# Kernel optimization log

Measured on AMD Instinct MI355X. Metric: run time of the kernel, lower is better.

## Reference

```python
import jax, jax.numpy as jnp
import numpy as np

BN_EPS = 1e-5

def setup_inputs() -> dict:
    key = jax.random.key(0)
    ks = jax.random.split(key, 4)
    B, C, H, W = 8, 64, 128, 128
    return {
        "x": jax.random.normal(ks[0], (B, C, H, W), jnp.float32),
        "w_reduce": jax.random.normal(ks[1], (C, C), jnp.float32) * 0.05,
        "b_reduce": jnp.zeros((C,), jnp.float32),
        "bn_gamma": jnp.ones((C,), jnp.float32),
        "bn_beta": jnp.zeros((C,), jnp.float32),
        "w_span": jax.random.normal(ks[2], (9, C), jnp.float32) * 0.05,
        "b_span": jnp.zeros((9,), jnp.float32),
        "w_conv2": jax.random.normal(ks[3], (C, C, 3, 3), jnp.float32) * 0.02,
        "b_conv2": jnp.zeros((C,), jnp.float32),
    }


def _involution(x, w_reduce, b_reduce, bn_gamma, bn_beta, w_span, b_span):
    # Involution2d: in_ch == out_ch so initial_mapping is Identity; groups=1, reduce_ratio=1, stride=1.
    B, C, H, W = x.shape
    # unfold 3x3, pad 1 -> patches [B, C, 9, H, W] (torch unfold ordering: C major, then kh, kw)
    xp = jnp.pad(x, ((0, 0), (0, 0), (1, 1), (1, 1)))
    patches = jnp.stack(
        [xp[:, :, i:i + H, j:j + W] for i in range(3) for j in range(3)], axis=2
    )  # [B, C, 9, H, W]
    # kernel generation: 1x1 conv -> BatchNorm2d (batch stats) -> ReLU -> 1x1 conv
    r = jnp.einsum('oc,bchw->bohw', w_reduce, x) + b_reduce[None, :, None, None]
    mu = r.mean(axis=(0, 2, 3), keepdims=True)
    var = r.var(axis=(0, 2, 3), keepdims=True)
    rn = (r - mu) * jax.lax.rsqrt(var + BN_EPS)
    rn = jax.nn.relu(rn * bn_gamma[None, :, None, None] + bn_beta[None, :, None, None])
    kern = jnp.einsum('kc,bchw->bkhw', w_span, rn) + b_span[None, :, None, None]  # [B, 9, H, W]
    # per-pixel dynamic kernel applied to patches, summed over kernel axis
    return jnp.einsum('bkhw,bckhw->bchw', kern, patches)


def reference(x, w_reduce, b_reduce, bn_gamma, bn_beta, w_span, b_span, w_conv2, b_conv2):
    z = jax.nn.softplus(_involution(x, w_reduce, b_reduce, bn_gamma, bn_beta, w_span, b_span))
    y = jax.lax.conv_general_dilated(z, w_conv2, window_strides=(1, 1), padding=((1, 1), (1, 1)))
    y = y + b_conv2[None, :, None, None]
    return jax.nn.softplus(y)
```

## Files before the change

### kernel.cpp

```cpp
#include <hip/hip_runtime.h>
#include <math.h>

#define H_ 128
#define W_ 128
#define C_ 64
#define B_ 8
#define HW 16384
#define NPIX (B_*HW)

typedef __attribute__((ext_vector_type(8))) short short8;
typedef __attribute__((ext_vector_type(4))) float f32x4;

__device__ __forceinline__ float softplus_fast(float v) {
    return fmaxf(v, 0.f) + __logf(1.f + __expf(-fabsf(v)));
}

__device__ __forceinline__ unsigned short f2bf(float f) {
    unsigned u = __builtin_bit_cast(unsigned, f);
    unsigned r = (u + 0x7fffu + ((u >> 16) & 1u)) >> 16;
    return (unsigned short)r;
}

__device__ __forceinline__ void gl_lds16(const float* g, float* l) {
    __builtin_amdgcn_global_load_lds(
        (const __attribute__((address_space(1))) void*)g,
        (__attribute__((address_space(3))) void*)l, 16, 0, 0);
}

__global__ __launch_bounds__(256) void k0_wtr(const float* __restrict__ w2,
                                              const float* __restrict__ wr,
                                              const float* __restrict__ wspan,
                                              unsigned short* __restrict__ wtr,
                                              unsigned short* __restrict__ wtr1,
                                              unsigned short* __restrict__ wtr2,
                                              float* __restrict__ stats)
{
    int t = blockIdx.x * 256 + threadIdx.x;
    if (t < 256) stats[t] = 0.f;
    if (t < 512) {
        int lane = t & 63, f = t >> 6;
        int mt = f >> 1, kh = f & 1;
        int o  = mt * 16 + (lane & 15);
        int c0 = kh * 32 + ((lane >> 4) << 3);
        uint4 pk;
        unsigned short* pv = (unsigned short*)&pk;
#pragma unroll
        for (int e = 0; e < 8; ++e)
            pv[e] = f2bf(wr[o * C_ + c0 + e]);
        *(uint4*)&wtr1[(size_t)t * 8] = pk;
    } else if (t < 640) {
        int tt = t - 512;
        int lane = tt & 63, kh = tt >> 6;
        int o  = lane & 15;
        int c0 = (kh << 5) + ((lane >> 4) << 3);
        uint4 pk;
        unsigned short* pv = (unsigned short*)&pk;
#pragma unroll
        for (int e = 0; e < 8; ++e)
            pv[e] = (o < 9) ? f2bf(wspan[o * C_ + c0 + e]) : (unsigned short)0;
        *(uint4*)&wtr2[(size_t)tt * 8] = pk;
    }
    if (t >= 4 * 18 * 64) return;
    int lane = t & 63;
    int f    = (t >> 6) % 18;
    int wv   = t / (18 * 64);
    int koff = f >> 1, ch = f & 1;
    int o = wv * 16 + (lane & 15);
    int cb = ch * 32 + ((lane >> 4) << 3);
    uint4 pk;
    unsigned short* pv = (unsigned short*)&pk;
#pragma unroll
    for (int e = 0; e < 8; ++e)
        pv[e] = f2bf(w2[(size_t)o * 576 + (size_t)(cb + e) * 9 + koff]);
    *(uint4*)&wtr[(size_t)t * 8] = pk;
}

__global__ __launch_bounds__(256) void k1_mfma(
    const float* __restrict__ x, const unsigned short* __restrict__ wtr1,
    const float* __restrict__ br, unsigned short* __restrict__ rb,
    float* __restrict__ stats)
{
    __shared__ unsigned short xb[256 * 64];
    __shared__ float brs[C_];
    __shared__ float ls[128];
    int tid = threadIdx.x;
    int blk = blockIdx.x;
    int pid0 = blk << 8;
    int b    = pid0 >> 14;
    int rem0 = pid0 & (HW - 1);
    const float* xbase = x + (((size_t)b * C_) << 14) + rem0;

    if (tid < C_) brs[tid] = br[tid];
    if (tid < 128) ls[tid] = 0.f;

    int p = tid;
#pragma unroll
    for (int m = 0; m < 8; ++m) {
        float tmp[8];
#pragma unroll
        for (int e = 0; e < 8; ++e)
            tmp[e] = xbase[((size_t)(m * 8 + e) << 14) + p];
        unsigned pk[4];
#pragma unroll
        for (int e = 0; e < 4; ++e)
            pk[e] = (unsigned)f2bf(tmp[2 * e]) | ((unsigned)f2bf(tmp[2 * e + 1]) << 16);
        *(uint4*)&xb[(p << 6) + ((m ^ (p & 7)) << 3)] = *(uint4*)pk;
    }

    int wid = tid >> 6, lane = tid & 63;
    int nl  = lane & 15;
    int kg  = lane >> 4;

    short8 af[8];
    const short8* wp = (const short8*)wtr1;
#pragma unroll
    for (int f = 0; f < 8; ++f) af[f] = wp[f * 64 + lane];

    f32x4 acc[4][4];
#pragma unroll
    for (int mt = 0; mt < 4; ++mt)
#pragma unroll
        for (int nt = 0; nt < 4; ++nt) acc[mt][nt] = (f32x4){0.f, 0.f, 0.f, 0.f};

    __syncthreads();

    int nbase = wid << 6;
#pragma unroll
    for (int nt = 0; nt < 4; ++nt) {
        int pp = nbase + (nt << 4) + nl;
#pragma unroll
        for (int kh = 0; kh < 2; ++kh) {
            int m = kh * 4 + kg;
            short8 bf = *(const short8*)&xb[(pp << 6) + ((m ^ (pp & 7)) << 3)];
#pragma unroll
            for (int mt = 0; mt < 4; ++mt)
                acc[mt][nt] = __builtin_amdgcn_mfma_f32_16x16x32_bf16(
                    af[mt * 2 + kh], bf, acc[mt][nt], 0, 0, 0);
        }
    }

    __syncthreads();

    float s_[16], q_[16];
#pragma unroll
    for (int i = 0; i < 16; ++i) { s_[i] = 0.f; q_[i] = 0.f; }

#pragma unroll
    for (int mt = 0; mt < 4; ++mt) {
        int c = (mt << 4) + (kg << 2);
        float b0 = brs[c], b1 = brs[c + 1], b2v = brs[c + 2], b3 = brs[c + 3];
        int chunk = c >> 3;
#pragma unroll
        for (int nt = 0; nt < 4; ++nt) {
            int pp = nbase + (nt << 4) + nl;
            f32x4 a = acc[mt][nt];
            float v0 = a[0] + b0, v1 = a[1] + b1, v2 = a[2] + b2v, v3 = a[3] + b3;
            s_[mt * 4 + 0] += v0; q_[mt * 4 + 0] += v0 * v0;
            s_[mt * 4 + 1] += v1; q_[mt * 4 + 1] += v1 * v1;
            s_[mt * 4 + 2] += v2; q_[mt * 4 + 2] += v2 * v2;
            s_[mt * 4 + 3] += v3; q_[mt * 4 + 3] += v3 * v3;
            unsigned lo = (unsigned)f2bf(v0) | ((unsigned)f2bf(v1) << 16);
            unsigned hi = (unsigned)f2bf(v2) | ((unsigned)f2bf(v3) << 16);
            unsigned* dst = (unsigned*)&xb[(pp << 6) + ((chunk ^ (pp & 7)) << 3) + ((kg & 1) << 2)];
            dst[0] = lo;
            dst[1] = hi;
        }
    }

#pragma unroll
    for (int i = 0; i < 16; ++i) {
#pragma unroll
        for (int m = 1; m <= 8; m <<= 1) {
            s_[i] += __shfl_xor(s_[i], m, 64);
            q_[i] += __shfl_xor(q_[i], m, 64);
        }
    }
    if (nl == 0) {
#pragma unroll
        for (int i = 0; i < 16; ++i) {
            int c = ((i >> 2) << 4) + (kg << 2) + (i & 3);
            atomicAdd(&ls[c], s_[i]);
            atomicAdd(&ls[64 + c], q_[i]);
        }
    }
    __syncthreads();
    if (tid < 128) atomicAdd(&stats[tid], ls[tid]);

    uint4* rp = (uint4*)(rb + ((size_t)(pid0 + p) << 6));
#pragma unroll
    for (int m = 0; m < 8; ++m)
        rp[m] = *(const uint4*)&xb[(p << 6) + ((m ^ (p & 7)) << 3)];
}

__global__ __launch_bounds__(512, 4) void k34_fused(
    const float* __restrict__ x, const unsigned short* __restrict__ rb,
    const float* __restrict__ stats, const float* __restrict__ gamma,
    const float* __restrict__ beta, const unsigned short* __restrict__ wtr2,
    const float* __restrict__ bspan, const unsigned short* __restrict__ wtr,
    const float* __restrict__ b2, float* __restrict__ out)
{
    __shared__ float xh0[8 * 20 * 24], xh1[8 * 20 * 24];
    __shared__ unsigned short zt[324 * 64];
    __shared__ float a_s[C_], c_s[C_];

    int tid = threadIdx.x;
    if (tid < C_) {
        float inv_n = 1.f / (float)NPIX;
        float mu  = stats[tid] * inv_n;
        float var = stats[C_ + tid] * inv_n - mu * mu;
        float is  = rsqrtf(var + 1e-5f);
        float a   = gamma[tid] * is;
        a_s[tid] = a;
        c_s[tid] = beta[tid] - mu * a;
    }

    int blk = blockIdx.x;
    int b = blk >> 6, t = blk & 63;
    int h0 = (t >> 3) << 4, w0 = (t & 7) << 4;
    const float* xb_ = x + (((size_t)b * C_) << 14);
    const float* zgz = stats + 128;

    int goff[2];
#pragma unroll
    for (int k = 0; k < 2; ++k) {
        int item = (k << 9) + tid;
        int c    = item / 120;
        int rem  = item - c * 120;
        int row  = rem / 6;
        int ii   = rem - row * 6;
        int gh   = h0 + row - 2;
        int gw   = w0 - 4 + (ii << 2);
        bool ok = (item < 960) && ((unsigned)gh < 128u) && ((unsigned)gw < 128u);
        goff[k] = ok ? ((c << 14) + (gh << 7) + gw) : -1;
    }

    auto stage = [&](int g, float* buf) {
#pragma unroll
        for (int k = 0; k < 2; ++k) {
            if (k == 0 || tid < 448) {
                int item = (k << 9) + tid;
                const float* src = (goff[k] >= 0) ? (xb_ + (g << 17) + goff[k]) : zgz;
                gl_lds16(src, buf + (item << 2));
            }
        }
    };

    int lane = tid & 63;
    int w_  = tid >> 6;
    int nl  = lane & 15;
    int kg  = lane >> 4;
    short8 af0 = ((const short8*)wtr2)[lane];
    short8 af1 = ((const short8*)wtr2)[64 + lane];

    stage(0, xh0);
    __syncthreads();
    stage(1, xh1);

    float aa[2][8], cc[2][8];
#pragma unroll
    for (int kh = 0; kh < 2; ++kh) {
        int cb = (kh << 5) + (kg << 3);
#pragma unroll
        for (int e = 0; e < 8; ++e) { aa[kh][e] = a_s[cb + e]; cc[kh][e] = c_s[cb + e]; }
    }

    float* kl = (float*)zt;
#pragma unroll
    for (int i3 = 0; i3 < 3; ++i3) {
        int col = w_ * 3 + i3;
        if (col < 21) {
            int hp = (col << 4) + nl;
            int py = hp / 18, px = hp - py * 18;
            int gh = h0 + py - 1, gw = w0 + px - 1;
            int ghc = min(max(gh, 0), 127), gwc = min(max(gw, 0), 127);
            int pid2 = (b << 14) + (ghc << 7) + gwc;
            f32x4 acc9 = (f32x4){0.f, 0.f, 0.f, 0.f};
#pragma unroll
            for (int kh = 0; kh < 2; ++kh) {
                uint4 rv = *(const uint4*)(rb + ((size_t)pid2 << 6) + (kh << 5) + (kg << 3));
                const unsigned* ru = (const unsigned*)&rv;
                unsigned po[4];
#pragma unroll
                for (int e2 = 0; e2 < 4; ++e2) {
                    float lo = __builtin_bit_cast(float, ru[e2] << 16);
                    float hi = __builtin_bit_cast(float, ru[e2] & 0xffff0000u);
                    float r0 = fmaxf(aa[kh][2 * e2]     * lo + cc[kh][2 * e2],     0.f);
                    float r1 = fmaxf(aa[kh][2 * e2 + 1] * hi + cc[kh][2 * e2 + 1], 0.f);
                    po[e2] = (unsigned)f2bf(r0) | ((unsigned)f2bf(r1) << 16);
                }
                short8 bfrag = __builtin_bit_cast(short8, *(uint4*)po);
                acc9 = __builtin_amdgcn_mfma_f32_16x16x32_bf16(
                    kh ? af1 : af0, bfrag, acc9, 0, 0, 0);
            }
#pragma unroll
            for (int e = 0; e < 4; ++e) {
                int rr = (kg << 2) + e;
                if (rr < 9) kl[hp * 9 + rr] = acc9[e];
            }
        }
    }
    __syncthreads();

    bool hasPix = tid < 324;
    float kern0[9];
    if (hasPix) {
#pragma unroll
        for (int k = 0; k < 9; ++k) kern0[k] = kl[tid * 9 + k] + bspan[k];
    }
    __syncthreads();

    int py0 = tid / 18, px0 = tid - py0 * 18;
    bool ib0 = hasPix && ((unsigned)(h0 + py0 - 1) < 128u) && ((unsigned)(w0 + px0 - 1) < 128u);

#pragma unroll 1
    for (int g = 0; g < 8; ++g) {
        if (g >= 1 && g < 7) stage(g + 1, (g & 1) ? xh0 : xh1);
        const float* xf = (g & 1) ? xh1 : xh0;
        if (hasPix) {
            unsigned pk[4];
            if (ib0) {
#pragma unroll
                for (int cp = 0; cp < 4; ++cp) {
                    const float* p0 = xf + (cp * 2) * 480 + py0 * 24 + px0 + 2;
                    const float* p1 = p0 + 480;
                    float acc0 = 0.f, acc1 = 0.f;
#pragma unroll
                    for (int i = 0; i < 3; ++i)
#pragma unroll
                        for (int j = 0; j < 3; ++j) {
                            float kv = kern0[i * 3 + j];
                            acc0 += kv * p0[i * 24 + j];
                            acc1 += kv * p1[i * 24 + j];
                        }
                    pk[cp] = (unsigned)f2bf(softplus_fast(acc0))
                           | ((unsigned)f2bf(softplus_fast(acc1)) << 16);
                }
            } else {
#pragma unroll
                for (int cp = 0; cp < 4; ++cp) pk[cp] = 0u;
            }
            *(uint4*)&zt[(tid << 6) + ((g ^ (tid & 7)) << 3)] = *(uint4*)pk;
        }
        __syncthreads();
    }

    int og = w_ & 3, yh = w_ >> 2;
    int ybase = yh << 3;
    f32x4 acc[8];
#pragma unroll
    for (int nt = 0; nt < 8; ++nt) acc[nt] = (f32x4){0.f, 0.f, 0.f, 0.f};

    const short8* wp = (const short8*)wtr;
#pragma unroll
    for (int kh = 0; kh < 2; ++kh) {
        short8 wfh[9];
#pragma unroll
        for (int f9 = 0; f9 < 9; ++f9)
            wfh[f9] = wp[(size_t)(og * 18 + f9 * 2 + kh) * 64 + lane];
        int cg = kh * 4 + kg;
#pragma unroll
        for (int yy = 0; yy < 10; ++yy) {
            int y = ybase + yy;
            short8 bf[3];
#pragma unroll
            for (int j = 0; j < 3; ++j) {
                int p = y * 18 + j + nl;
                bf[j] = *(const short8*)&zt[(p << 6) + ((cg ^ (p & 7)) << 3)];
            }
#pragma unroll
            for (int i = 0; i < 3; ++i) {
                int nt = yy - i;
                if (nt >= 0 && nt < 8) {
#pragma unroll
                    for (int j = 0; j < 3; ++j)
                        acc[nt] = __builtin_amdgcn_mfma_f32_16x16x32_bf16(
                            wfh[i * 3 + j], bf[j], acc[nt], 0, 0, 0);
                }
            }
        }
    }

    float bias[4];
#pragma unroll
    for (int r = 0; r < 4; ++r) bias[r] = b2[(og << 4) + (kg << 2) + r];

    size_t ob = ((size_t)b) << 20;
#pragma unroll
    for (int nt = 0; nt < 8; ++nt) {
        int h = h0 + ybase + nt;
#pragma unroll
        for (int r = 0; r < 4; ++r) {
            int o = (og << 4) + (kg << 2) + r;
            float v = acc[nt][r] + bias[r];
            out[ob + ((size_t)o << 14) + (h << 7) + w0 + nl] = softplus_fast(v);
        }
    }
}

extern "C" void kernel_launch(void* const* d_in, const int* in_sizes, int n_in,
                              void* d_out, int out_size, void* d_ws, size_t ws_size,
                              hipStream_t stream)
{
    const float* x   = (const float*)d_in[0];
    const float* wr  = (const float*)d_in[1];
    const float* br  = (const float*)d_in[2];
    const float* gam = (const float*)d_in[3];
    const float* bet = (const float*)d_in[4];
    const float* wsp = (const float*)d_in[5];
    const float* bsp = (const float*)d_in[6];
    const float* w2  = (const float*)d_in[7];
    const float* b2  = (const float*)d_in[8];
    float* out = (float*)d_out;

    unsigned short* rb   = (unsigned short*)d_ws;
    unsigned short* wtr  = rb + (size_t)NPIX * C_;
    unsigned short* wtr1 = wtr + 4608 * 8;
    unsigned short* wtr2 = wtr1 + 512 * 8;
    float* stats = (float*)(wtr2 + 128 * 8);

    k0_wtr<<<18, 256, 0, stream>>>(w2, wr, wsp, wtr, wtr1, wtr2, stats);
    k1_mfma<<<NPIX / 256, 256, 0, stream>>>(x, wtr1, br, rb, stats);
    k34_fused<<<NPIX / 256, 512, 0, stream>>>(x, rb, stats, gam, bet, wtr2, bsp,
                                              wtr, b2, out);
}
```

Measured before the change: 76.90 us.

## Stage involution input as channel-last bf16 copy written by reduce kernel

```diff
diff --git a/kernel.cpp b/kernel.cpp
--- a/kernel.cpp
+++ b/kernel.cpp
@@ -21,7 +21,14 @@
     return (unsigned short)r;
 }
 
-__device__ __forceinline__ void gl_lds16(const float* g, float* l) {
+__device__ __forceinline__ float bf_lo(unsigned u) {
+    return __builtin_bit_cast(float, u << 16);
+}
+__device__ __forceinline__ float bf_hi(unsigned u) {
+    return __builtin_bit_cast(float, u & 0xffff0000u);
+}
+
+__device__ __forceinline__ void gl_lds16(const void* g, void* l) {
     __builtin_amdgcn_global_load_lds(
         (const __attribute__((address_space(1))) void*)g,
         (__attribute__((address_space(3))) void*)l, 16, 0, 0);
@@ -78,7 +85,7 @@
 __global__ __launch_bounds__(256) void k1_mfma(
     const float* __restrict__ x, const unsigned short* __restrict__ wtr1,
     const float* __restrict__ br, unsigned short* __restrict__ rb,
-    float* __restrict__ stats)
+    unsigned short* __restrict__ xq, float* __restrict__ stats)
 {
     __shared__ unsigned short xb[256 * 64];
     __shared__ float brs[C_];
@@ -137,6 +144,13 @@
                 acc[mt][nt] = __builtin_amdgcn_mfma_f32_16x16x32_bf16(
                     af[mt * 2 + kh], bf, acc[mt][nt], 0, 0, 0);
         }
+    }
+
+    {
+        uint4* xp = (uint4*)(xq + ((size_t)(pid0 + p) << 6));
+#pragma unroll
+        for (int m = 0; m < 8; ++m)
+            xp[m] = *(const uint4*)&xb[(p << 6) + ((m ^ (p & 7)) << 3)];
     }
 
     __syncthreads();
@@ -193,13 +207,13 @@
 }
 
 __global__ __launch_bounds__(512, 4) void k34_fused(
-    const float* __restrict__ x, const unsigned short* __restrict__ rb,
+    const unsigned short* __restrict__ xq, const unsigned short* __restrict__ rb,
     const float* __restrict__ stats, const float* __restrict__ gamma,
     const float* __restrict__ beta, const unsigned short* __restrict__ wtr2,
     const float* __restrict__ bspan, const unsigned short* __restrict__ wtr,
     const float* __restrict__ b2, float* __restrict__ out)
 {
-    __shared__ float xh0[8 * 20 * 24], xh1[8 * 20 * 24];
+    __shared__ unsigned short xh0[400 * 8], xh1[400 * 8];
     __shared__ unsigned short zt[324 * 64];
     __shared__ float a_s[C_], c_s[C_];
 
@@ -217,31 +231,21 @@
     int blk = blockIdx.x;
     int b = blk >> 6, t = blk & 63;
     int h0 = (t >> 3) << 4, w0 = (t & 7) << 4;
-    const float* xb_ = x + (((size_t)b * C_) << 14);
-    const float* zgz = stats + 128;
-
-    int goff[2];
-#pragma unroll
-    for (int k = 0; k < 2; ++k) {
-        int item = (k << 9) + tid;
-        int c    = item / 120;
-        int rem  = item - c * 120;
-        int row  = rem / 6;
-        int ii   = rem - row * 6;
-        int gh   = h0 + row - 2;
-        int gw   = w0 - 4 + (ii << 2);
-        bool ok = (item < 960) && ((unsigned)gh < 128u) && ((unsigned)gw < 128u);
-        goff[k] = ok ? ((c << 14) + (gh << 7) + gw) : -1;
-    }
-
-    auto stage = [&](int g, float* buf) {
-#pragma unroll
-        for (int k = 0; k < 2; ++k) {
-            if (k == 0 || tid < 448) {
-                int item = (k << 9) + tid;
-                const float* src = (goff[k] >= 0) ? (xb_ + (g << 17) + goff[k]) : zgz;
-                gl_lds16(src, buf + (item << 2));
-            }
+    const unsigned short* xqb = xq + (((size_t)b) << 20);
+    const unsigned short* zgz = (const unsigned short*)(stats + 128);
+
+    int gq = -1;
+    if (tid < 400) {
+        int hr = tid / 20, hc = tid - hr * 20;
+        int gh = h0 + hr - 2, gw = w0 + hc - 2;
+        if ((unsigned)gh < 128u && (unsigned)gw < 128u) gq = (gh << 7) + gw;
+    }
+
+    auto stage = [&](int g, unsigned short* buf) {
+        if (tid < 400) {
+            const unsigned short* src = (gq >= 0)
+                ? (xqb + (((size_t)gq) << 6) + (g << 3)) : zgz;
+            gl_lds16(src, buf + (tid << 3));
         }
     };
 
@@ -282,8 +286,8 @@
                 unsigned po[4];
 #pragma unroll
                 for (int e2 = 0; e2 < 4; ++e2) {
-                    float lo = __builtin_bit_cast(float, ru[e2] << 16);
-                    float hi = __builtin_bit_cast(float, ru[e2] & 0xffff0000u);
+                    float lo = bf_lo(ru[e2]);
+                    float hi = bf_hi(ru[e2]);
                     float r0 = fmaxf(aa[kh][2 * e2]     * lo + cc[kh][2 * e2],     0.f);
                     float r1 = fmaxf(aa[kh][2 * e2 + 1] * hi + cc[kh][2 * e2 + 1], 0.f);
                     po[e2] = (unsigned)f2bf(r0) | ((unsigned)f2bf(r1) << 16);
@@ -311,30 +315,35 @@
 
     int py0 = tid / 18, px0 = tid - py0 * 18;
     bool ib0 = hasPix && ((unsigned)(h0 + py0 - 1) < 128u) && ((unsigned)(w0 + px0 - 1) < 128u);
+    int hbase = py0 * 20 + px0;
 
 #pragma unroll 1
     for (int g = 0; g < 8; ++g) {
         if (g >= 1 && g < 7) stage(g + 1, (g & 1) ? xh0 : xh1);
-        const float* xf = (g & 1) ? xh1 : xh0;
+        const unsigned short* xf = (g & 1) ? xh1 : xh0;
         if (hasPix) {
             unsigned pk[4];
             if (ib0) {
-#pragma unroll
-                for (int cp = 0; cp < 4; ++cp) {
-                    const float* p0 = xf + (cp * 2) * 480 + py0 * 24 + px0 + 2;
-                    const float* p1 = p0 + 480;
-                    float acc0 = 0.f, acc1 = 0.f;
-#pragma unroll
-                    for (int i = 0; i < 3; ++i)
-#pragma unroll
-                        for (int j = 0; j < 3; ++j) {
-                            float kv = kern0[i * 3 + j];
-                            acc0 += kv * p0[i * 24 + j];
-                            acc1 += kv * p1[i * 24 + j];
+                float az[8];
+#pragma unroll
+                for (int e = 0; e < 8; ++e) az[e] = 0.f;
+#pragma unroll
+                for (int i = 0; i < 3; ++i)
+#pragma unroll
+                    for (int j = 0; j < 3; ++j) {
+                        uint4 tv = *(const uint4*)&xf[(hbase + i * 20 + j) << 3];
+                        const unsigned* tu = (const unsigned*)&tv;
+                        float kv = kern0[i * 3 + j];
+#pragma unroll
+                        for (int e2 = 0; e2 < 4; ++e2) {
+                            az[2 * e2]     += kv * bf_lo(tu[e2]);
+                            az[2 * e2 + 1] += kv * bf_hi(tu[e2]);
                         }
-                    pk[cp] = (unsigned)f2bf(softplus_fast(acc0))
-                           | ((unsigned)f2bf(softplus_fast(acc1)) << 16);
-                }
+                    }
+#pragma unroll
+                for (int cp = 0; cp < 4; ++cp)
+                    pk[cp] = (unsigned)f2bf(softplus_fast(az[2 * cp]))
+                           | ((unsigned)f2bf(softplus_fast(az[2 * cp + 1])) << 16);
             } else {
 #pragma unroll
                 for (int cp = 0; cp < 4; ++cp) pk[cp] = 0u;
@@ -413,13 +422,14 @@
     float* out = (float*)d_out;
 
     unsigned short* rb   = (unsigned short*)d_ws;
-    unsigned short* wtr  = rb + (size_t)NPIX * C_;
+    unsigned short* xq   = rb + (size_t)NPIX * C_;
+    unsigned short* wtr  = xq + (size_t)NPIX * C_;
     unsigned short* wtr1 = wtr + 4608 * 8;
     unsigned short* wtr2 = wtr1 + 512 * 8;
     float* stats = (float*)(wtr2 + 128 * 8);
 
     k0_wtr<<<18, 256, 0, stream>>>(w2, wr, wsp, wtr, wtr1, wtr2, stats);
-    k1_mfma<<<NPIX / 256, 256, 0, stream>>>(x, wtr1, br, rb, stats);
-    k34_fused<<<NPIX / 256, 512, 0, stream>>>(x, rb, stats, gam, bet, wtr2, bsp,
+    k1_mfma<<<NPIX / 256, 256, 0, stream>>>(x, wtr1, br, rb, xq, stats);
+    k34_fused<<<NPIX / 256, 512, 0, stream>>>(xq, rb, stats, gam, bet, wtr2, bsp,
                                               wtr, b2, out);
 }
```

After: 78.76 us. 1.02x slower.
